# Performance work log

Measured on AMD Instinct MI355X. Metric: run time of the kernel, lower is better.

## Reference

```python
import jax, jax.numpy as jnp
import numpy as np

N, E, U, EF, STEPS = 5000, 40000, 64, 16, 4


def setup_inputs() -> dict:
    key = jax.random.key(0)
    ks = jax.random.split(key, 7)
    node_features = jax.random.normal(ks[0], (N, U), dtype=jnp.float32)
    edge_features = jax.random.normal(ks[1], (E, EF), dtype=jnp.float32)
    pair_indices = jax.random.randint(ks[2], (E, 2), 0, N, dtype=jnp.int32)
    # EdgeNetwork params: kernel (efc, nfc*nfc), bias (nfc*nfc,)
    edge_kernel = jax.random.normal(ks[3], (EF, U * U), dtype=jnp.float32) * 0.05
    edge_bias = jnp.zeros((U * U,), dtype=jnp.float32)
    # Keras GRUCell (reset_after=True): kernel (in, 3u), recurrent (u, 3u), bias (2, 3u)
    gru_kernel = jax.random.normal(ks[4], (U, 3 * U), dtype=jnp.float32) * 0.05
    gru_recurrent_kernel = jax.random.normal(ks[5], (U, 3 * U), dtype=jnp.float32) * 0.05
    gru_bias = jnp.zeros((2, 3 * U), dtype=jnp.float32)
    return {
        "node_features": node_features,
        "edge_features": edge_features,
        "pair_indices": pair_indices,
        "edge_kernel": edge_kernel,
        "edge_bias": edge_bias,
        "gru_kernel": gru_kernel,
        "gru_recurrent_kernel": gru_recurrent_kernel,
        "gru_bias": gru_bias,
    }


def _gru_cell(x, h, kernel, rkernel, bias):
    # Keras GRUCell math with reset_after=True
    u = h.shape[-1]
    mx = x @ kernel + bias[0]          # [N, 3u]
    mh = h @ rkernel + bias[1]         # [N, 3u]
    xz, xr, xh = mx[:, :u], mx[:, u:2 * u], mx[:, 2 * u:]
    iz, ir, ih = mh[:, :u], mh[:, u:2 * u], mh[:, 2 * u:]
    z = jax.nn.sigmoid(xz + iz)
    r = jax.nn.sigmoid(xr + ir)
    hh = jnp.tanh(xh + r * ih)
    return z * h + (1.0 - z) * hh


def reference(node_features, edge_features, pair_indices, edge_kernel, edge_bias,
              gru_kernel, gru_recurrent_kernel, gru_bias):
    n = node_features.shape[0]
    u = node_features.shape[1]  # units (pad_length = 0 since nfc == units)
    src = pair_indices[:, 0]
    nbr = pair_indices[:, 1]
    # Edge matrices are loop-invariant: [E, u, u]
    edge_mats = (edge_features @ edge_kernel + edge_bias).reshape(-1, u, u)
    h = node_features
    for _ in range(STEPS):
        nb = h[nbr]                                    # gather [E, u]
        msg = jnp.einsum('eij,ej->ei', edge_mats, nb)  # per-edge matvec
        agg = jax.ops.segment_sum(msg, src, num_segments=n)  # scatter-sum [N, u]
        h = _gru_cell(agg, h, gru_kernel, gru_recurrent_kernel, gru_bias)
    return h
```

## Files before the change

kernel.cpp:

```cpp
#include <hip/hip_runtime.h>
#include <math.h>

#define NN 5000
#define NE 40000
#define UU 64
#define FE 16
#define FEP 17
#define KD (FEP*UU)
#define KH2 (KD/2)
#define LDK (KD+8)
#define NSTEPS 4
#define NT 16
#define NB ((NN+NT-1)/NT)
#define SLOT 40
#define CH 8
#define WBN (UU*KD)
#define GTN (192*64)

typedef _Float16 half8 __attribute__((ext_vector_type(8)));
typedef float f32x4 __attribute__((ext_vector_type(4)));

__device__ __forceinline__ float sigm(float x){ return 1.f/(1.f + __expf(-x)); }
__device__ __forceinline__ int rfl(int x){ return __builtin_amdgcn_readfirstlane(x); }

__global__ void build_k(const float* __restrict__ ek, const float* __restrict__ eb,
                        const float* __restrict__ gk, const float* __restrict__ rk,
                        _Float16* __restrict__ wb, _Float16* __restrict__ gkt,
                        _Float16* __restrict__ rkt, int* __restrict__ deg){
  int tid = blockIdx.x*blockDim.x + threadIdx.x;
  if (tid < NN) deg[tid] = 0;
  if (tid < WBN){
    int i = tid / KD, k = tid - i*KD;
    int f = k >> 6, j = k & 63;
    float v = (f < FE) ? ek[f*4096 + i*64 + j] : eb[i*64 + j];
    wb[tid] = (_Float16)v;
  } else if (tid < WBN + GTN){
    int r = tid - WBN; int n = r >> 6, k = r & 63;
    gkt[r] = (_Float16)gk[k*192 + n];
  } else if (tid < WBN + 2*GTN){
    int r = tid - WBN - GTN; int n = r >> 6, k = r & 63;
    rkt[r] = (_Float16)rk[k*192 + n];
  }
}

__global__ void bucket_k(const int* __restrict__ pair, int* __restrict__ deg,
                         int* __restrict__ eidb){
  int e = blockIdx.x*blockDim.x + threadIdx.x;
  if (e < NE){
    int v = pair[2*e];
    int pos = atomicAdd(&deg[v], 1);
    if (pos < SLOT) eidb[v*SLOT + pos] = e;
  }
}

__global__ __launch_bounds__(512) void prep_k(const int* __restrict__ pair,
                       const int* __restrict__ deg,
                       const int* __restrict__ eidb, int2* __restrict__ enb){
  int w = threadIdx.x >> 6, lane = threadIdx.x & 63;
  int v = blockIdx.x * 8 + w;
  if (v >= NN) return;
  int dg = deg[v]; if (dg > SLOT) dg = SLOT;
  if (lane < dg){
    int e = eidb[v*SLOT + lane];
    int rank = 0;
    for (int j=0; j<dg; ++j){ int ej = eidb[v*SLOT + j]; rank += (ej < e); }
    enb[v*SLOT + rank] = make_int2(e, pair[2*e + 1]);
  }
}

__global__ __launch_bounds__(512) void step_k(const float* __restrict__ h_in,
        float* __restrict__ h_out, const float* __restrict__ ef,
        const int* __restrict__ deg, const int2* __restrict__ enb,
        const _Float16* __restrict__ wb, const _Float16* __restrict__ gkt,
        const _Float16* __restrict__ rkt, const float* __restrict__ gb){
  __shared__ _Float16 Gs[NT*LDK];
  __shared__ float    aggP[2][16][68];
  __shared__ _Float16 aggT[16*72];
  __shared__ _Float16 hT[16*72];

  int tid = threadIdx.x;
  int w = tid >> 6, lane = tid & 63;
  int r16 = lane & 15, kh = lane >> 4;
  int vb = blockIdx.x * NT;

  for (int i=tid; i<NT*64; i+=512){
    int lv = i >> 6, j = i & 63; int v = vb + lv;
    hT[lv*72 + j] = (_Float16)((v < NN) ? h_in[(size_t)v*64 + j] : 0.f);
  }

  {
    int v0 = vb + w*2, v1 = v0 + 1;
    int d0 = (v0 < NN) ? deg[v0] : 0; if (d0 > SLOT) d0 = SLOT; d0 = rfl(d0);
    int d1 = (v1 < NN) ? deg[v1] : 0; if (d1 > SLOT) d1 = SLOT; d1 = rfl(d1);
    const int2* l0 = enb + (size_t)v0*SLOT;
    const int2* l1 = enb + (size_t)v1*SLOT;
    float gA[FEP], gB[FEP];
    #pragma unroll
    for (int f=0;f<FEP;++f){ gA[f] = 0.f; gB[f] = 0.f; }
    int dmax = (d0 > d1) ? d0 : d1;
    for (int c0=0; c0<dmax; c0+=CH){
      int eA[CH], nA[CH], eB[CH], nB[CH];
      #pragma unroll
      for (int q=0;q<CH;++q){ int i=c0+q;
        if (i<d0){ int2 p = l0[i]; eA[q]=rfl(p.x); nA[q]=rfl(p.y); }
        else { eA[q]=0; nA[q]=0; }
        if (i<d1){ int2 p = l1[i]; eB[q]=rfl(p.x); nB[q]=rfl(p.y); }
        else { eB[q]=0; nB[q]=0; } }
      float hA[CH], hB[CH];
      #pragma unroll
      for (int q=0;q<CH;++q){ int i=c0+q;
        hA[q] = (i<d0) ? h_in[(size_t)nA[q]*64 + lane] : 0.f;
        hB[q] = (i<d1) ? h_in[(size_t)nB[q]*64 + lane] : 0.f; }
      #pragma unroll
      for (int q=0;q<CH;++q){ int i=c0+q;
        if (i<d0){
          const float4* er = (const float4*)(ef + (size_t)eA[q]*FE);
          float4 e0 = er[0], e1 = er[1], e2 = er[2], e3 = er[3];
          float hj = hA[q];
          gA[ 0]=fmaf(e0.x,hj,gA[ 0]); gA[ 1]=fmaf(e0.y,hj,gA[ 1]);
          gA[ 2]=fmaf(e0.z,hj,gA[ 2]); gA[ 3]=fmaf(e0.w,hj,gA[ 3]);
          gA[ 4]=fmaf(e1.x,hj,gA[ 4]); gA[ 5]=fmaf(e1.y,hj,gA[ 5]);
          gA[ 6]=fmaf(e1.z,hj,gA[ 6]); gA[ 7]=fmaf(e1.w,hj,gA[ 7]);
          gA[ 8]=fmaf(e2.x,hj,gA[ 8]); gA[ 9]=fmaf(e2.y,hj,gA[ 9]);
          gA[10]=fmaf(e2.z,hj,gA[10]); gA[11]=fmaf(e2.w,hj,gA[11]);
          gA[12]=fmaf(e3.x,hj,gA[12]); gA[13]=fmaf(e3.y,hj,gA[13]);
          gA[14]=fmaf(e3.z,hj,gA[14]); gA[15]=fmaf(e3.w,hj,gA[15]);
          gA[16] += hj;
        }
        if (i<d1){
          const float4* er = (const float4*)(ef + (size_t)eB[q]*FE);
          float4 e0 = er[0], e1 = er[1], e2 = er[2], e3 = er[3];
          float hj = hB[q];
          gB[ 0]=fmaf(e0.x,hj,gB[ 0]); gB[ 1]=fmaf(e0.y,hj,gB[ 1]);
          gB[ 2]=fmaf(e0.z,hj,gB[ 2]); gB[ 3]=fmaf(e0.w,hj,gB[ 3]);
          gB[ 4]=fmaf(e1.x,hj,gB[ 4]); gB[ 5]=fmaf(e1.y,hj,gB[ 5]);
          gB[ 6]=fmaf(e1.z,hj,gB[ 6]); gB[ 7]=fmaf(e1.w,hj,gB[ 7]);
          gB[ 8]=fmaf(e2.x,hj,gB[ 8]); gB[ 9]=fmaf(e2.y,hj,gB[ 9]);
          gB[10]=fmaf(e2.z,hj,gB[10]); gB[11]=fmaf(e2.w,hj,gB[11]);
          gB[12]=fmaf(e3.x,hj,gB[12]); gB[13]=fmaf(e3.y,hj,gB[13]);
          gB[14]=fmaf(e3.z,hj,gB[14]); gB[15]=fmaf(e3.w,hj,gB[15]);
          gB[16] += hj;
        } }
    }
    #pragma unroll
    for (int f=0;f<FEP;++f){
      Gs[(w*2  )*LDK + f*64 + lane] = (_Float16)gA[f];
      Gs[(w*2+1)*LDK + f*64 + lane] = (_Float16)gB[f];
    }
  }
  __syncthreads();

  {
    int cg = w & 3, khalf = w >> 2;
    int koff = khalf * KH2;
    f32x4 acc = {0.f,0.f,0.f,0.f};
    const _Float16* ap = Gs + r16*LDK + koff + kh*8;
    const _Float16* bp = wb + (size_t)(cg*16 + r16)*KD + koff + kh*8;
    #pragma unroll 4
    for (int k0=0; k0<KH2; k0+=32){
      half8 a = *(const half8*)(ap + k0);
      half8 b = *(const half8*)(bp + k0);
      acc = __builtin_amdgcn_mfma_f32_16x16x32_f16(a, b, acc, 0, 0, 0);
    }
    #pragma unroll
    for (int r=0;r<4;++r) aggP[khalf][kh*4+r][cg*16 + r16] = acc[r];
  }
  __syncthreads();

  for (int i=tid; i<NT*64; i+=512){
    int rw = i >> 6, cl = i & 63;
    aggT[rw*72 + cl] = (_Float16)(aggP[0][rw][cl] + aggP[1][rw][cl]);
  }
  __syncthreads();

  if (w < 4){
    int uw = w*16 + r16;
    const _Float16* az = aggT + r16*72 + kh*8;
    const _Float16* ah = hT   + r16*72 + kh*8;
    f32x4 mxz={0.f,0.f,0.f,0.f}, mxr=mxz, mxh=mxz, mhz=mxz, mhr=mxz, mhh=mxz;
    #pragma unroll
    for (int ks=0; ks<2; ++ks){
      half8 aa = *(const half8*)(az + ks*32);
      half8 hh = *(const half8*)(ah + ks*32);
      half8 bz = *(const half8*)(gkt + (size_t)(      uw)*64 + ks*32 + kh*8);
      half8 br = *(const half8*)(gkt + (size_t)( 64 + uw)*64 + ks*32 + kh*8);
      half8 bh = *(const half8*)(gkt + (size_t)(128 + uw)*64 + ks*32 + kh*8);
      half8 cz = *(const half8*)(rkt + (size_t)(      uw)*64 + ks*32 + kh*8);
      half8 cr = *(const half8*)(rkt + (size_t)( 64 + uw)*64 + ks*32 + kh*8);
      half8 ch = *(const half8*)(rkt + (size_t)(128 + uw)*64 + ks*32 + kh*8);
      mxz = __builtin_amdgcn_mfma_f32_16x16x32_f16(aa, bz, mxz, 0,0,0);
      mxr = __builtin_amdgcn_mfma_f32_16x16x32_f16(aa, br, mxr, 0,0,0);
      mxh = __builtin_amdgcn_mfma_f32_16x16x32_f16(aa, bh, mxh, 0,0,0);
      mhz = __builtin_amdgcn_mfma_f32_16x16x32_f16(hh, cz, mhz, 0,0,0);
      mhr = __builtin_amdgcn_mfma_f32_16x16x32_f16(hh, cr, mhr, 0,0,0);
      mhh = __builtin_amdgcn_mfma_f32_16x16x32_f16(hh, ch, mhh, 0,0,0);
    }
    float b0z = gb[uw],      b0r = gb[64+uw],  b0h = gb[128+uw];
    float b1z = gb[192+uw],  b1r = gb[256+uw], b1h = gb[320+uw];
    #pragma unroll
    for (int r=0;r<4;++r){
      int row = vb + kh*4 + r;
      if (row < NN){
        float z  = sigm(mxz[r] + b0z + mhz[r] + b1z);
        float rr = sigm(mxr[r] + b0r + mhr[r] + b1r);
        float hc = tanhf(mxh[r] + b0h + rr*(mhh[r] + b1h));
        float hold = h_in[(size_t)row*64 + uw];
        h_out[(size_t)row*64 + uw] = z*hold + (1.f - z)*hc;
      }
    }
  }
}

extern "C" void kernel_launch(void* const* d_in, const int* in_sizes, int n_in,
                              void* d_out, int out_size, void* d_ws, size_t ws_size,
                              hipStream_t stream){
  const float* nodef = (const float*)d_in[0];
  const float* edgef = (const float*)d_in[1];
  const int*   pair  = (const int*)  d_in[2];
  const float* ek    = (const float*)d_in[3];
  const float* ebias = (const float*)d_in[4];
  const float* gk    = (const float*)d_in[5];
  const float* rk    = (const float*)d_in[6];
  const float* gb    = (const float*)d_in[7];

  char* ws = (char*)d_ws;
  size_t o = 0;
  auto carve = [&](size_t bytes)->char*{
    char* p = ws + o; o = (o + bytes + 255) & ~255ULL; return p; };
  int*      deg  = (int*)     carve(NN*sizeof(int));
  int*      eidb = (int*)     carve((size_t)NN*SLOT*sizeof(int));
  int2*     enb  = (int2*)    carve((size_t)NN*SLOT*sizeof(int2));
  _Float16* wb   = (_Float16*)carve((size_t)WBN*sizeof(_Float16));
  _Float16* gkt  = (_Float16*)carve((size_t)GTN*sizeof(_Float16));
  _Float16* rkt  = (_Float16*)carve((size_t)GTN*sizeof(_Float16));
  float*    hA   = (float*)   carve((size_t)NN*UU*sizeof(float));
  float*    hB   = (float*)   carve((size_t)NN*UU*sizeof(float));

  build_k <<<(WBN+2*GTN+255)/256, 256, 0, stream>>>(ek, ebias, gk, rk, wb, gkt, rkt, deg);
  bucket_k<<<(NE+255)/256, 256, 0, stream>>>(pair, deg, eidb);
  prep_k  <<<(NN+7)/8, 512, 0, stream>>>(pair, deg, eidb, enb);

  const float* hin = nodef;
  for (int s=0; s<NSTEPS; ++s){
    float* hout = (s == NSTEPS-1) ? (float*)d_out : ((s & 1) ? hB : hA);
    step_k<<<NB, 512, 0, stream>>>(hin, hout, edgef, deg, enb,
                                   wb, gkt, rkt, gb);
    hin = hout;
  }
}
```

Before: 116.0 us.

## Halve node tile to 8 per block with 256-thread blocks and drop K-split

Each block now handles 8 nodes with 4 waves instead of 16 nodes with 8 waves, doubling the grid to 625 blocks for better CU coverage. The edge-matrix MFMA no longer splits K across two wave halves, so the partial-sum buffer, its reduction pass and one barrier go away. Each wave now runs the full K loop over wb, and half of every 16-row MFMA tile is wasted on duplicated rows. The h staging is folded into the gather phase and the bounds checks are dropped, since 5000 divides evenly by 8.

```diff
diff --git a/kernel.cpp b/kernel.cpp
--- a/kernel.cpp
+++ b/kernel.cpp
@@ -7,11 +7,10 @@
 #define FE 16
 #define FEP 17
 #define KD (FEP*UU)
-#define KH2 (KD/2)
 #define LDK (KD+8)
 #define NSTEPS 4
-#define NT 16
-#define NB ((NN+NT-1)/NT)
+#define NT 8
+#define NB (NN/NT)
 #define SLOT 40
 #define CH 8
 #define WBN (UU*KD)
@@ -68,30 +67,26 @@
   }
 }
 
-__global__ __launch_bounds__(512) void step_k(const float* __restrict__ h_in,
+__global__ __launch_bounds__(256) void step_k(const float* __restrict__ h_in,
         float* __restrict__ h_out, const float* __restrict__ ef,
         const int* __restrict__ deg, const int2* __restrict__ enb,
         const _Float16* __restrict__ wb, const _Float16* __restrict__ gkt,
         const _Float16* __restrict__ rkt, const float* __restrict__ gb){
   __shared__ _Float16 Gs[NT*LDK];
-  __shared__ float    aggP[2][16][68];
-  __shared__ _Float16 aggT[16*72];
-  __shared__ _Float16 hT[16*72];
+  __shared__ _Float16 aggT[NT*72];
+  __shared__ _Float16 hT[NT*72];
 
   int tid = threadIdx.x;
   int w = tid >> 6, lane = tid & 63;
   int r16 = lane & 15, kh = lane >> 4;
   int vb = blockIdx.x * NT;
 
-  for (int i=tid; i<NT*64; i+=512){
-    int lv = i >> 6, j = i & 63; int v = vb + lv;
-    hT[lv*72 + j] = (_Float16)((v < NN) ? h_in[(size_t)v*64 + j] : 0.f);
-  }
-
   {
     int v0 = vb + w*2, v1 = v0 + 1;
-    int d0 = (v0 < NN) ? deg[v0] : 0; if (d0 > SLOT) d0 = SLOT; d0 = rfl(d0);
-    int d1 = (v1 < NN) ? deg[v1] : 0; if (d1 > SLOT) d1 = SLOT; d1 = rfl(d1);
+    hT[(w*2  )*72 + lane] = (_Float16)h_in[(size_t)v0*64 + lane];
+    hT[(w*2+1)*72 + lane] = (_Float16)h_in[(size_t)v1*64 + lane];
+    int d0 = rfl(deg[v0]); if (d0 > SLOT) d0 = SLOT;
+    int d1 = rfl(deg[v1]); if (d1 > SLOT) d1 = SLOT;
     const int2* l0 = enb + (size_t)v0*SLOT;
     const int2* l1 = enb + (size_t)v1*SLOT;
     float gA[FEP], gB[FEP];
@@ -151,32 +146,26 @@
   __syncthreads();
 
   {
-    int cg = w & 3, khalf = w >> 2;
-    int koff = khalf * KH2;
     f32x4 acc = {0.f,0.f,0.f,0.f};
-    const _Float16* ap = Gs + r16*LDK + koff + kh*8;
-    const _Float16* bp = wb + (size_t)(cg*16 + r16)*KD + koff + kh*8;
+    const _Float16* ap = Gs + (r16 & 7)*LDK + kh*8;
+    const _Float16* bp = wb + (size_t)(w*16 + r16)*KD + kh*8;
     #pragma unroll 4
-    for (int k0=0; k0<KH2; k0+=32){
+    for (int k0=0; k0<KD; k0+=32){
       half8 a = *(const half8*)(ap + k0);
       half8 b = *(const half8*)(bp + k0);
       acc = __builtin_amdgcn_mfma_f32_16x16x32_f16(a, b, acc, 0, 0, 0);
     }
-    #pragma unroll
-    for (int r=0;r<4;++r) aggP[khalf][kh*4+r][cg*16 + r16] = acc[r];
+    if (kh < 2){
+      #pragma unroll
+      for (int r=0;r<4;++r) aggT[(kh*4+r)*72 + w*16 + r16] = (_Float16)acc[r];
+    }
   }
   __syncthreads();
 
-  for (int i=tid; i<NT*64; i+=512){
-    int rw = i >> 6, cl = i & 63;
-    aggT[rw*72 + cl] = (_Float16)(aggP[0][rw][cl] + aggP[1][rw][cl]);
-  }
-  __syncthreads();
-
-  if (w < 4){
+  {
     int uw = w*16 + r16;
-    const _Float16* az = aggT + r16*72 + kh*8;
-    const _Float16* ah = hT   + r16*72 + kh*8;
+    const _Float16* az = aggT + (r16 & 7)*72 + kh*8;
+    const _Float16* ah = hT   + (r16 & 7)*72 + kh*8;
     f32x4 mxz={0.f,0.f,0.f,0.f}, mxr=mxz, mxh=mxz, mhz=mxz, mhr=mxz, mhh=mxz;
     #pragma unroll
     for (int ks=0; ks<2; ++ks){
@@ -195,12 +184,12 @@
       mhr = __builtin_amdgcn_mfma_f32_16x16x32_f16(hh, cr, mhr, 0,0,0);
       mhh = __builtin_amdgcn_mfma_f32_16x16x32_f16(hh, ch, mhh, 0,0,0);
     }
-    float b0z = gb[uw],      b0r = gb[64+uw],  b0h = gb[128+uw];
-    float b1z = gb[192+uw],  b1r = gb[256+uw], b1h = gb[320+uw];
-    #pragma unroll
-    for (int r=0;r<4;++r){
-      int row = vb + kh*4 + r;
-      if (row < NN){
+    if (kh < 2){
+      float b0z = gb[uw],      b0r = gb[64+uw],  b0h = gb[128+uw];
+      float b1z = gb[192+uw],  b1r = gb[256+uw], b1h = gb[320+uw];
+      #pragma unroll
+      for (int r=0;r<4;++r){
+        int row = vb + kh*4 + r;
         float z  = sigm(mxz[r] + b0z + mhz[r] + b1z);
         float rr = sigm(mxr[r] + b0r + mhr[r] + b1r);
         float hc = tanhf(mxh[r] + b0h + rr*(mhh[r] + b1h));
@@ -238,12 +227,12 @@
 
   build_k <<<(WBN+2*GTN+255)/256, 256, 0, stream>>>(ek, ebias, gk, rk, wb, gkt, rkt, deg);
   bucket_k<<<(NE+255)/256, 256, 0, stream>>>(pair, deg, eidb);
-  prep_k  <<<(NN+7)/8, 512, 0, stream>>>(pair, deg, eidb, enb);
+  prep_k  <<<NB, 512, 0, stream>>>(pair, deg, eidb, enb);
 
   const float* hin = nodef;
   for (int s=0; s<NSTEPS; ++s){
     float* hout = (s == NSTEPS-1) ? (float*)d_out : ((s & 1) ? hB : hA);
-    step_k<<<NB, 512, 0, stream>>>(hin, hout, edgef, deg, enb,
+    step_k<<<NB, 256, 0, stream>>>(hin, hout, edgef, deg, enb,
                                    wb, gkt, rkt, gb);
     hin = hout;
   }
```

Result: slower. 126.6 us (+9.1%).
